# Kernel tuning notes

Hardware: AMD Instinct MI355X
Metric: run time of the kernel (lower is better)

Reference implementation:

```python
import jax, jax.numpy as jnp
import numpy as np

B, S, D = 16, 2048, 768  # batch, padded subword length, roberta hidden dim


def setup_inputs() -> dict:
    key = jax.random.key(0)
    k1, k2 = jax.random.split(key)
    robert_embed = jax.random.normal(k1, (B, S, D), dtype=jnp.float32)
    # Non-decreasing per-row segment ids: contiguous runs of equal ids are the
    # subword spans that merge_list would average; singleton runs pass through.
    seg_ids = jnp.sort(jax.random.randint(k2, (B, S), 0, S, dtype=jnp.int32), axis=-1)
    return {"robert_embed": robert_embed, "seg_ids": seg_ids}


def reference(robert_embed, seg_ids):
    # Segment-mean gather/scatter: out[b, w] = mean_{p: seg_ids[b,p]==w} x[b, p]
    b, s, d = robert_embed.shape
    w = s  # output word slots (<= s); empty slots yield zeros
    flat_seg = (seg_ids + (w * jnp.arange(b, dtype=seg_ids.dtype))[:, None]).reshape(-1)
    x_flat = robert_embed.reshape(-1, d)
    sums = jax.ops.segment_sum(x_flat, flat_seg, num_segments=b * w)  # [b*w, d]
    counts = jax.ops.segment_sum(
        jnp.ones((b * s,), dtype=robert_embed.dtype), flat_seg, num_segments=b * w
    )
    out = sums / jnp.maximum(counts, 1)[:, None]
    return out.reshape(b, w, d)
```

## Files before the change

kernel.cpp:

```cpp
#include <hip/hip_runtime.h>

#define BB 16
#define SS 2048
#define DD 768
#define D4 (DD / 4)

__global__ void seg_prep(const int* __restrict__ seg,
                         int* __restrict__ counts,
                         int* __restrict__ starts) {
    int idx = blockIdx.x * blockDim.x + threadIdx.x;
    if (idx >= BB * SS) return;
    int p = idx & (SS - 1);
    int s = seg[idx];
    int base = (idx - p);
    atomicAdd(&counts[base + s], 1);
    if (p == 0 || seg[idx - 1] != s) starts[base + s] = p;
}

__global__ __launch_bounds__(64) void seg_mean(const float* __restrict__ x,
                                               const int* __restrict__ counts,
                                               const int* __restrict__ starts,
                                               float* __restrict__ out) {
    int bw = blockIdx.x;
    int t  = threadIdx.x;
    int c  = counts[bw];

    float4* outp = (float4*)(out + (size_t)bw * DD);
    if (c == 0) {
        float4 z = make_float4(0.f, 0.f, 0.f, 0.f);
        outp[t]       = z;
        outp[t + 64]  = z;
        outp[t + 128] = z;
        return;
    }

    int b  = bw >> 11;
    int st = starts[bw];
    const float4* xp = (const float4*)(x + ((size_t)b * SS + (size_t)st) * DD);

    float4 a0 = xp[t];
    float4 a1 = xp[t + 64];
    float4 a2 = xp[t + 128];
    for (int j = 1; j < c; ++j) {
        const float4* xr = xp + (size_t)j * D4;
        float4 r0 = xr[t], r1 = xr[t + 64], r2 = xr[t + 128];
        a0.x += r0.x; a0.y += r0.y; a0.z += r0.z; a0.w += r0.w;
        a1.x += r1.x; a1.y += r1.y; a1.z += r1.z; a1.w += r1.w;
        a2.x += r2.x; a2.y += r2.y; a2.z += r2.z; a2.w += r2.w;
    }
    float inv = 1.0f / (float)c;
    a0.x *= inv; a0.y *= inv; a0.z *= inv; a0.w *= inv;
    a1.x *= inv; a1.y *= inv; a1.z *= inv; a1.w *= inv;
    a2.x *= inv; a2.y *= inv; a2.z *= inv; a2.w *= inv;
    outp[t]       = a0;
    outp[t + 64]  = a1;
    outp[t + 128] = a2;
}

extern "C" void kernel_launch(void* const* d_in, const int* in_sizes, int n_in,
                              void* d_out, int out_size, void* d_ws, size_t ws_size,
                              hipStream_t stream) {
    const float* x   = (const float*)d_in[0];
    const int*   seg = (const int*)d_in[1];
    float* out = (float*)d_out;

    int* counts = (int*)d_ws;
    int* starts = counts + BB * SS;

    hipMemsetAsync(counts, 0, (size_t)BB * SS * sizeof(int), stream);

    int nPos = BB * SS;
    seg_prep<<<(nPos + 255) / 256, 256, 0, stream>>>(seg, counts, starts);
    seg_mean<<<nPos, 64, 0, stream>>>(x, counts, starts, out);
}
```

Before: 183.3 us.

## Fuse segment prep into mean kernel via per-wave binary search and ballot

Drops the memset and the atomic-count prep kernel. Each wavefront now finds its segment start by binary-searching the sorted seg row and counts the run length with a ballot scan. Four output slots are packed per 256-thread block instead of one per 64-thread block, which cuts the block count. The cost is some redundant seg reads per wave, though these are small and cache-resident.

```diff
diff --git a/kernel.cpp b/kernel.cpp
--- a/kernel.cpp
+++ b/kernel.cpp
@@ -5,45 +5,52 @@
 #define DD 768
 #define D4 (DD / 4)
 
-__global__ void seg_prep(const int* __restrict__ seg,
-                         int* __restrict__ counts,
-                         int* __restrict__ starts) {
-    int idx = blockIdx.x * blockDim.x + threadIdx.x;
-    if (idx >= BB * SS) return;
-    int p = idx & (SS - 1);
-    int s = seg[idx];
-    int base = (idx - p);
-    atomicAdd(&counts[base + s], 1);
-    if (p == 0 || seg[idx - 1] != s) starts[base + s] = p;
-}
+__global__ __launch_bounds__(256) void seg_mean_fused(
+    const float* __restrict__ x,
+    const int*   __restrict__ seg,
+    float*       __restrict__ out) {
+    int lane = threadIdx.x & 63;
+    int wave = threadIdx.x >> 6;
+    int bw   = (blockIdx.x << 2) + wave;
+    int b    = bw >> 11;
+    int w    = bw & (SS - 1);
+    const int* srow = seg + (b << 11);
 
-__global__ __launch_bounds__(64) void seg_mean(const float* __restrict__ x,
-                                               const int* __restrict__ counts,
-                                               const int* __restrict__ starts,
-                                               float* __restrict__ out) {
-    int bw = blockIdx.x;
-    int t  = threadIdx.x;
-    int c  = counts[bw];
+    int lo = 0, n = SS;
+    while (n > 0) {
+        int half = n >> 1;
+        int mid  = lo + half;
+        if (srow[mid] < w) { lo = mid + 1; n -= half + 1; }
+        else               { n = half; }
+    }
+
+    int c = 0;
+    int p = lo;
+    for (;;) {
+        int idx = p + lane;
+        int v   = (idx < SS) ? srow[idx] : -1;
+        unsigned long long m = __ballot(v == w);
+        unsigned long long nm = ~m;
+        if (nm) { c += (int)__builtin_ctzll(nm); break; }
+        c += 64; p += 64;
+    }
 
     float4* outp = (float4*)(out + (size_t)bw * DD);
     if (c == 0) {
         float4 z = make_float4(0.f, 0.f, 0.f, 0.f);
-        outp[t]       = z;
-        outp[t + 64]  = z;
-        outp[t + 128] = z;
+        outp[lane]       = z;
+        outp[lane + 64]  = z;
+        outp[lane + 128] = z;
         return;
     }
 
-    int b  = bw >> 11;
-    int st = starts[bw];
-    const float4* xp = (const float4*)(x + ((size_t)b * SS + (size_t)st) * DD);
-
-    float4 a0 = xp[t];
-    float4 a1 = xp[t + 64];
-    float4 a2 = xp[t + 128];
+    const float4* xp = (const float4*)(x + ((size_t)b * SS + (size_t)lo) * DD);
+    float4 a0 = xp[lane];
+    float4 a1 = xp[lane + 64];
+    float4 a2 = xp[lane + 128];
     for (int j = 1; j < c; ++j) {
         const float4* xr = xp + (size_t)j * D4;
-        float4 r0 = xr[t], r1 = xr[t + 64], r2 = xr[t + 128];
+        float4 r0 = xr[lane], r1 = xr[lane + 64], r2 = xr[lane + 128];
         a0.x += r0.x; a0.y += r0.y; a0.z += r0.z; a0.w += r0.w;
         a1.x += r1.x; a1.y += r1.y; a1.z += r1.z; a1.w += r1.w;
         a2.x += r2.x; a2.y += r2.y; a2.z += r2.z; a2.w += r2.w;
@@ -52,9 +59,9 @@
     a0.x *= inv; a0.y *= inv; a0.z *= inv; a0.w *= inv;
     a1.x *= inv; a1.y *= inv; a1.z *= inv; a1.w *= inv;
     a2.x *= inv; a2.y *= inv; a2.z *= inv; a2.w *= inv;
-    outp[t]       = a0;
-    outp[t + 64]  = a1;
-    outp[t + 128] = a2;
+    outp[lane]       = a0;
+    outp[lane + 64]  = a1;
+    outp[lane + 128] = a2;
 }
 
 extern "C" void kernel_launch(void* const* d_in, const int* in_sizes, int n_in,
@@ -64,12 +71,6 @@
     const int*   seg = (const int*)d_in[1];
     float* out = (float*)d_out;
 
-    int* counts = (int*)d_ws;
-    int* starts = counts + BB * SS;
-
-    hipMemsetAsync(counts, 0, (size_t)BB * SS * sizeof(int), stream);
-
-    int nPos = BB * SS;
-    seg_prep<<<(nPos + 255) / 256, 256, 0, stream>>>(seg, counts, starts);
-    seg_mean<<<nPos, 64, 0, stream>>>(x, counts, starts, out);
+    int nBlocks = (BB * SS) / 4;
+    seg_mean_fused<<<nBlocks, 256, 0, stream>>>(x, seg, out);
 }
```

After: 180.6 us. Within noise of the previous version (-1.5%).
